# Kernel tuning notes

Hardware: AMD Instinct MI355X
Metric: run time of the kernel (lower is better)

The kernel has to match this reference:

```python
import jax, jax.numpy as jnp
import numpy as np

EPS = 1e-12  # matches torch F.normalize eps

def l2norm(x):
    n = jnp.linalg.norm(x, axis=-1, keepdims=True)
    return x / jnp.maximum(n, EPS)

def setup_inputs() -> dict:
    key = jax.random.key(0)
    ks = jax.random.split(key, 5)
    B, T, A, D, H = 32, 512, 64, 128, 256
    actions = jax.random.normal(ks[0], (B, T, A), dtype=jnp.float32)
    init_structure = jax.random.normal(ks[1], (D,), dtype=jnp.float32)
    # MLP params (scaled like typical init)
    w1 = jax.random.normal(ks[2], (A, H), dtype=jnp.float32) / jnp.sqrt(A)
    b1 = jnp.zeros((H,), dtype=jnp.float32)
    w2 = jax.random.normal(ks[3], (H, D * D), dtype=jnp.float32) / jnp.sqrt(H)
    b2 = jnp.zeros((D * D,), dtype=jnp.float32)
    return {"actions": actions, "init_structure": init_structure,
            "w1": w1, "b1": b1, "w2": w2, "b2": b2}

def reference(actions, init_structure, w1, b1, w2, b2):
    B, T, A = actions.shape
    D = init_structure.shape[0]
    # MLP: actions -> transition matrices [B, T, D, D]
    h = jax.nn.relu(jnp.einsum('bta,ah->bth', actions, w1) + b1)
    trans = (jnp.einsum('bth,hk->btk', h, w2) + b2).reshape(B, T, D, D)
    # initial structure, l2-normalized and broadcast over batch
    s0 = jnp.broadcast_to(l2norm(init_structure), (B, D))
    # sequential recurrence over time
    def step(s, Tm):  # s: [B, D], Tm: [B, D, D]
        s = jax.nn.relu(jnp.einsum('bi,bij->bj', s, Tm))
        s = l2norm(s)
        return s, s
    _, ys = jax.lax.scan(step, s0, jnp.swapaxes(trans, 0, 1))  # ys: [T, B, D]
    return jnp.swapaxes(ys, 0, 1)  # [B, T, D]
```

## Files before the change

### kernel.cpp

```cpp
#include <hip/hip_runtime.h>
#include <stdint.h>
#include <math.h>


typedef _Float16 f16x8 __attribute__((ext_vector_type(8)));
typedef float    f32x4 __attribute__((ext_vector_type(4)));

#define B_  32
#define T_  512
#define A_  64
#define H_  256
#define D_  128
#define N_  (D_ * D_)
#define M_  (B_ * T_)

__device__ inline void glds(const void* g, void* l) {
  __builtin_amdgcn_global_load_lds(
      (__attribute__((address_space(1))) void*)g,
      (__attribute__((address_space(3))) void*)l, 16, 0, 0);
}

__global__ __launch_bounds__(256) void w2cast_kernel(const float* __restrict__ w2,
                                                     _Float16* __restrict__ w2t) {
  __shared__ float tile[64][65];
  const int t = threadIdx.x;
  const int n0 = blockIdx.x * 64, k0 = blockIdx.y * 64;
  const int nn = t & 63, kg = t >> 6;
  #pragma unroll
  for (int r = 0; r < 16; ++r) {
    int k = kg * 16 + r;
    tile[k][nn] = w2[(size_t)(k0 + k) * N_ + n0 + nn];
  }
  __syncthreads();
  const int kk = t & 63, ng = t >> 6;
  #pragma unroll
  for (int r = 0; r < 16; ++r) {
    int n = ng * 16 + r;
    int ngl = n0 + n;
    int i = ngl >> 7, j = ngl & 127;
    int p = ((j >> 4) << 11) | ((i >> 5) << 9) | (((i >> 3) & 3) << 7)
          | ((j & 15) << 3) | (i & 7);
    w2t[(size_t)p * H_ + k0 + kk] = (_Float16)tile[kk][n];
  }
}

__global__ __launch_bounds__(256) void h_kernel(const float* __restrict__ actions,
                                                const float* __restrict__ w1,
                                                const float* __restrict__ b1,
                                                _Float16* __restrict__ h16) {
  __shared__ float w1s[32 * 256];
  __shared__ float acts[32 * 64];
  const int t = threadIdx.x;
  const size_t row0 = (size_t)blockIdx.x * 32;

  #pragma unroll
  for (int i = 0; i < 8; ++i) acts[t + i * 256] = actions[row0 * A_ + t + i * 256];

  float acc[32];
  float bj = b1[t];
  #pragma unroll
  for (int r = 0; r < 32; ++r) acc[r] = bj;

  for (int half = 0; half < 2; ++half) {
    __syncthreads();
    #pragma unroll
    for (int i = 0; i < 32; ++i) w1s[t + i * 256] = w1[half * 32 * 256 + t + i * 256];
    __syncthreads();
    #pragma unroll
    for (int r = 0; r < 32; ++r) {
      float a = acc[r];
      #pragma unroll
      for (int k = 0; k < 32; ++k)
        a += acts[r * 64 + half * 32 + k] * w1s[k * 256 + t];
      acc[r] = a;
    }
  }
  #pragma unroll
  for (int r = 0; r < 32; ++r)
    h16[(row0 + r) * H_ + t] = (_Float16)fmaxf(acc[r], 0.f);
}

__global__ __launch_bounds__(512, 2) void fused_kernel(
    const _Float16* __restrict__ h16, const _Float16* __restrict__ w2t,
    const float* __restrict__ b2, _Float16* __restrict__ tbuf0,
    _Float16* __restrict__ tbuf1, const float* __restrict__ init_s,
    float* __restrict__ out, float* __restrict__ dummyws,
    int Tc, int tcs, int c, int nch) {

  __shared__ __align__(16) char smem[33536];
  const int tid  = threadIdx.x;
  const int lane = tid & 63;
  const int w    = tid >> 6;

  if (blockIdx.x < 32) {
    if (c < 0) return;
    const char* trans = (const char*)((c & 1) ? tbuf1 : tbuf0);
    const int b  = blockIdx.x;
    const int t0 = c * Tc;
    const int n16 = lane & 15, q = lane >> 4;
    const int col = w * 16 + n16;
    const int Tcm1 = Tc - 1;
    float* red = (float*)(smem + 33280);
    _Float16* sb0p = (_Float16*)(smem + 32768);

    float v0 = 0.f;
    if (tid < 128) {
      v0 = (t0 == 0) ? init_s[tid] : out[((size_t)b * T_ + t0 - 1) * D_ + tid];
      float ss = v0 * v0;
      #pragma unroll
      for (int off = 32; off > 0; off >>= 1) ss += __shfl_xor(ss, off);
      if (lane == 0) red[w] = ss;
    }
    __syncthreads();
    if (tid < 128) {
      float inv0 = 1.f / fmaxf(sqrtf(red[0] + red[1]), 1e-12f);
      sb0p[tid] = (_Float16)(v0 * inv0);
    }
    __syncthreads();

    float uprev = (float)sb0p[col];

    const unsigned sbase = (unsigned)(size_t)(__attribute__((address_space(3))) char*)smem;
    const unsigned aA0 = sbase + 32768 + q * 16;
    const unsigned aA1 = sbase + 33024 + q * 16;
    const unsigned aW0 = sbase + 33024 + col * 2;
    const unsigned aW1 = sbase + 32768 + col * 2;
    const char* Gw = trans + (size_t)b * Tc * 32768 + w * 4096 + lane * 16;
    float* outb = out + (size_t)b * T_ * D_ + col;
    float* dsink = dummyws + blockIdx.x * 128 + col;

    f16x8 ring[4][4];
#define LDSLOT(S, P)                                                          \
    asm volatile("global_load_dwordx4 %0, %4, off\n\t"                        \
                 "global_load_dwordx4 %1, %4, off offset:1024\n\t"            \
                 "global_load_dwordx4 %2, %4, off offset:2048\n\t"            \
                 "global_load_dwordx4 %3, %4, off offset:3072"                \
                 : "=v"(ring[S][0]), "=v"(ring[S][1]),                        \
                   "=v"(ring[S][2]), "=v"(ring[S][3])                         \
                 : "v"(P) : "memory")
    LDSLOT(0, Gw + 0 * 32768);
    LDSLOT(1, Gw + 1 * 32768);
    LDSLOT(2, Gw + 2 * 32768);
    LDSLOT(3, Gw + 3 * 32768);

    const f32x4 zf = {0.f, 0.f, 0.f, 0.f};

#define STEP(TT, PAR, SPAR, WAITN)                                            \
    {                                                                         \
      const int tt = (TT);                                                    \
      f16x8 A0, A1, A2, A3;                                                   \
      asm volatile(                                                           \
        "s_waitcnt vmcnt(" #WAITN ")\n\t"                                     \
        "ds_read_b128 %0, %8 offset:0\n\t"                                    \
        "ds_read_b128 %1, %8 offset:64\n\t"                                   \
        "ds_read_b128 %2, %8 offset:128\n\t"                                  \
        "ds_read_b128 %3, %8 offset:192\n\t"                                  \
        "s_waitcnt lgkmcnt(0)"                                                \
        : "=v"(A0), "=v"(A1), "=v"(A2), "=v"(A3),                             \
          "+v"(ring[PAR][0]), "+v"(ring[PAR][1]),                             \
          "+v"(ring[PAR][2]), "+v"(ring[PAR][3])                              \
        : "v"(aA##SPAR) : "memory");                                          \
      f32x4 c0 = __builtin_amdgcn_mfma_f32_16x16x32_f16(A0, ring[PAR][0], zf, 0, 0, 0); \
      f32x4 c1 = __builtin_amdgcn_mfma_f32_16x16x32_f16(A1, ring[PAR][1], zf, 0, 0, 0); \
      f32x4 c2 = __builtin_amdgcn_mfma_f32_16x16x32_f16(A2, ring[PAR][2], zf, 0, 0, 0); \
      f32x4 c3 = __builtin_amdgcn_mfma_f32_16x16x32_f16(A3, ring[PAR][3], zf, 0, 0, 0); \
      f32x4 cs = __builtin_amdgcn_mfma_f32_16x16x32_f16(A0, A0, zf, 0, 0, 0); \
      cs = __builtin_amdgcn_mfma_f32_16x16x32_f16(A1, A1, cs, 0, 0, 0);       \
      cs = __builtin_amdgcn_mfma_f32_16x16x32_f16(A2, A2, cs, 0, 0, 0);       \
      cs = __builtin_amdgcn_mfma_f32_16x16x32_f16(A3, A3, cs, 0, 0, 0);       \
      const char* gd = Gw + (size_t)((tt + 4) & Tcm1) * 32768;                \
      LDSLOT(PAR, gd);                                                        \
      float ssp = cs[0];                                                      \
      float inv = 1.f / fmaxf(sqrtf(ssp), 1e-12f);                            \
      float y = c0[0] + c1[0] + c2[0] + c3[0];                                \
      float un = fmaxf(y, 0.f) * inv;                                         \
      float o = uprev * inv;                                                  \
      uprev = un;                                                             \
      _Float16 hv = (_Float16)un;                                             \
      const int gt = t0 + tt;                                                 \
      float* gp = (gt > 0) ? (outb + (size_t)(gt - 1) * D_) : dsink;          \
      asm volatile("ds_write_b16 %0, %1\n\t"                                  \
                   "global_store_dword %2, %3, off"                           \
                   :: "v"(aW##SPAR), "v"(hv), "v"(gp), "v"(o) : "memory");    \
      asm volatile("s_waitcnt lgkmcnt(0)\n\ts_barrier" ::: "memory");         \
    }

    STEP(0, 0, 0, 12)
    STEP(1, 1, 1, 13)
    STEP(2, 2, 0, 14)
    STEP(3, 3, 1, 15)
    for (int tt0 = 4; tt0 < Tc; tt0 += 4) {
      STEP(tt0,     0, 0, 16)
      STEP(tt0 + 1, 1, 1, 16)
      STEP(tt0 + 2, 2, 0, 16)
      STEP(tt0 + 3, 3, 1, 16)
    }
#undef STEP
#undef LDSLOT
    asm volatile("s_waitcnt vmcnt(0)" ::: "memory");

    {
      float x = 0.f;
      if (lane < 16) x = (float)((_Float16*)(smem + 32768))[col];
      float ss2 = x * x;
      ss2 += __shfl_xor(ss2, 1);
      ss2 += __shfl_xor(ss2, 2);
      ss2 += __shfl_xor(ss2, 4);
      ss2 += __shfl_xor(ss2, 8);
      if (lane == 0) red[w] = ss2;
      __syncthreads();
      float tot = 0.f;
      #pragma unroll
      for (int g = 0; g < 8; ++g) tot += red[g];
      float inv = 1.f / fmaxf(sqrtf(tot), 1e-12f);
      if (lane < 16) outb[(size_t)(t0 + Tc - 1) * D_] = uprev * inv;
    }
  } else {
    const int g = c + 1;
    if (g >= nch) return;
    _Float16* trans = (g & 1) ? tbuf1 : tbuf0;
    const int t0g = g * Tc;

    _Float16* smA = (_Float16*)smem;
    _Float16* smB = (_Float16*)(smem + 16384);

    const int wm = w >> 2, wn = w & 3;
    const int fm = lane & 15, fq = lane >> 4;
    const f32x4 zero = {0.f, 0.f, 0.f, 0.f};

    const int cA0 = tid, cA1 = tid + 512;
    const int rA0 = cA0 >> 2, kA0 = cA0 & 3;
    const int rA1 = cA1 >> 2, kA1 = cA1 & 3;

    const int mtiles = (B_ * Tc) >> 8;
    const int ntot = mtiles * 64;
    for (int tile = (int)blockIdx.x - 32; tile < ntot; tile += 224) {
      const int bn = tile & 63;
      const int bm = tile >> 6;

      const int mc0 = bm * 256 + rA0, mc1 = bm * 256 + rA1;
      const int bb0 = mc0 >> tcs, bb1 = mc1 >> tcs;
      const _Float16* gA0 = h16 + ((size_t)bb0 * T_ + t0g + (mc0 & (Tc - 1))) * H_ + kA0 * 8;
      const _Float16* gA1 = h16 + ((size_t)bb1 * T_ + t0g + (mc1 & (Tc - 1))) * H_ + kA1 * 8;
      const _Float16* gB0 = w2t + ((size_t)bn * 256 + rA0) * H_ + kA0 * 8;
      const _Float16* gB1 = w2t + ((size_t)bn * 256 + rA1) * H_ + kA1 * 8;
      _Float16* lA0 = &smA[cA0 * 8];
      _Float16* lA1 = &smA[cA1 * 8];
      _Float16* lB0 = &smB[cA0 * 8];
      _Float16* lB1 = &smB[cA1 * 8];

      f32x4 acc[8][4];
      #pragma unroll
      for (int i = 0; i < 8; ++i)
        #pragma unroll
        for (int j = 0; j < 4; ++j) acc[i][j] = zero;

      for (int kt = 0; kt < H_ / 32; ++kt) {
        __syncthreads();
        glds(gA0 + kt * 32, lA0);
        glds(gA1 + kt * 32, lA1);
        glds(gB0 + kt * 32, lB0);
        glds(gB1 + kt * 32, lB1);
        __syncthreads();
        f16x8 af[8], bf[4];
        #pragma unroll
        for (int mt = 0; mt < 8; ++mt)
          af[mt] = *(const f16x8*)&smA[(wm * 128 + mt * 16 + fm) * 32 + fq * 8];
        #pragma unroll
        for (int nt = 0; nt < 4; ++nt)
          bf[nt] = *(const f16x8*)&smB[(wn * 64 + nt * 16 + fm) * 32 + fq * 8];
        #pragma unroll
        for (int mt = 0; mt < 8; ++mt)
          #pragma unroll
          for (int nt = 0; nt < 4; ++nt)
            acc[mt][nt] = __builtin_amdgcn_mfma_f32_16x16x32_f16(af[mt], bf[nt], acc[mt][nt], 0, 0, 0);
      }

      #pragma unroll
      for (int nt = 0; nt < 4; ++nt) {
        int col = bn * 256 + wn * 64 + nt * 16 + fm;
        int pw = col >> 11, pf = (col >> 9) & 3, pq = (col >> 7) & 3;
        int pn = (col >> 3) & 15, pr = col & 7;
        int ii = pf * 32 + pq * 8 + pr, jj = pw * 16 + pn;
        float bias = b2[ii * 128 + jj];
        #pragma unroll
        for (int mt = 0; mt < 8; ++mt) {
          #pragma unroll
          for (int r = 0; r < 4; ++r) {
            long row = bm * 256 + wm * 128 + mt * 16 + fq * 4 + r;
            trans[row * (long)N_ + col] = (_Float16)(acc[mt][nt][r] + bias);
          }
        }
      }
      __syncthreads();
    }
  }
}

extern "C" void kernel_launch(void* const* d_in, const int* in_sizes, int n_in,
                              void* d_out, int out_size, void* d_ws, size_t ws_size,
                              hipStream_t stream) {
  const float* actions = (const float*)d_in[0];
  const float* init_s  = (const float*)d_in[1];
  const float* w1      = (const float*)d_in[2];
  const float* b1      = (const float*)d_in[3];
  const float* w2      = (const float*)d_in[4];
  const float* b2      = (const float*)d_in[5];
  float* out = (float*)d_out;

  uint8_t* ws = (uint8_t*)d_ws;
  _Float16* w2t = (_Float16*)ws;
  _Float16* h16 = (_Float16*)(ws + ((size_t)8 << 20));
  const size_t trans_off = (size_t)16 << 20;

  int Tc = 16;
  const int cands[3] = {64, 32, 16};
  for (int i = 0; i < 3; ++i) {
    if (trans_off + 2 * ((size_t)cands[i] << 20) + 65536 <= ws_size) { Tc = cands[i]; break; }
  }
  const int tcs = __builtin_ctz(Tc);
  _Float16* tbuf0 = (_Float16*)(ws + trans_off);
  _Float16* tbuf1 = (_Float16*)(ws + trans_off + ((size_t)Tc << 20));
  float* dummyws = (float*)(ws + trans_off + 2 * ((size_t)Tc << 20));

  w2cast_kernel<<<dim3(N_ / 64, 4), 256, 0, stream>>>(w2, w2t);
  h_kernel<<<M_ / 32, 256, 0, stream>>>(actions, w1, b1, h16);

  const int nch = T_ / Tc;
  for (int c = -1; c < nch; ++c) {
    fused_kernel<<<256, 512, 0, stream>>>(
        h16, w2t, b2, tbuf0, tbuf1, init_s, out, dummyws, Tc, tcs, c, nch);
  }
}
```

Before: 523.1 us.

## Replace per-chunk kernel launches with a persistent kernel using global flag synchronization

Collapses the loop of per-chunk fused_kernel launches into a single persistent launch. Recurrence blocks spin on per-group counters that the GEMM producer blocks increment once their tiles are written, and producers wait on consumer-done counters before reusing a double buffer. The aim is to remove launch gaps and the implicit grid-wide barrier between chunks, so producers can run ahead as far as the double buffer allows. In exchange it relies on all 256 blocks being co-resident and on correct memory fences, and spin-waiting adds polling overhead and deadlock risk.

```diff
diff --git a/kernel.cpp b/kernel.cpp
--- a/kernel.cpp
+++ b/kernel.cpp
@@ -21,7 +21,12 @@
 }
 
 __global__ __launch_bounds__(256) void w2cast_kernel(const float* __restrict__ w2,
-                                                     _Float16* __restrict__ w2t) {
+                                                     _Float16* __restrict__ w2t,
+                                                     unsigned* __restrict__ flags) {
+  if (blockIdx.x == 0 && blockIdx.y == 0) {
+    #pragma unroll
+    for (int i = 0; i < 4; ++i) flags[threadIdx.x + i * 256] = 0u;
+  }
   __shared__ float tile[64][65];
   const int t = threadIdx.x;
   const int n0 = blockIdx.x * 64, k0 = blockIdx.y * 64;
@@ -85,18 +90,16 @@
     const float* __restrict__ b2, _Float16* __restrict__ tbuf0,
     _Float16* __restrict__ tbuf1, const float* __restrict__ init_s,
     float* __restrict__ out, float* __restrict__ dummyws,
-    int Tc, int tcs, int c, int nch) {
+    unsigned* __restrict__ flags, int Tc, int tcs, int nch) {
 
   __shared__ __align__(16) char smem[33536];
   const int tid  = threadIdx.x;
   const int lane = tid & 63;
   const int w    = tid >> 6;
+  const int MT   = 1 << (tcs - 3);
 
   if (blockIdx.x < 32) {
-    if (c < 0) return;
-    const char* trans = (const char*)((c & 1) ? tbuf1 : tbuf0);
     const int b  = blockIdx.x;
-    const int t0 = c * Tc;
     const int n16 = lane & 15, q = lane >> 4;
     const int col = w * 16 + n16;
     const int Tcm1 = Tc - 1;
@@ -105,7 +108,7 @@
 
     float v0 = 0.f;
     if (tid < 128) {
-      v0 = (t0 == 0) ? init_s[tid] : out[((size_t)b * T_ + t0 - 1) * D_ + tid];
+      v0 = init_s[tid];
       float ss = v0 * v0;
       #pragma unroll
       for (int off = 32; off > 0; off >>= 1) ss += __shfl_xor(ss, off);
@@ -117,7 +120,6 @@
       sb0p[tid] = (_Float16)(v0 * inv0);
     }
     __syncthreads();
-
     float uprev = (float)sb0p[col];
 
     const unsigned sbase = (unsigned)(size_t)(__attribute__((address_space(3))) char*)smem;
@@ -125,11 +127,13 @@
     const unsigned aA1 = sbase + 33024 + q * 16;
     const unsigned aW0 = sbase + 33024 + col * 2;
     const unsigned aW1 = sbase + 32768 + col * 2;
-    const char* Gw = trans + (size_t)b * Tc * 32768 + w * 4096 + lane * 16;
     float* outb = out + (size_t)b * T_ * D_ + col;
-    float* dsink = dummyws + blockIdx.x * 128 + col;
+    float* dsink = dummyws + b * 128 + col;
+    const int grp = b >> (8 - tcs);
 
     f16x8 ring[4][4];
+    const f32x4 zf = {0.f, 0.f, 0.f, 0.f};
+
 #define LDSLOT(S, P)                                                          \
     asm volatile("global_load_dwordx4 %0, %4, off\n\t"                        \
                  "global_load_dwordx4 %1, %4, off offset:1024\n\t"            \
@@ -138,12 +142,6 @@
                  : "=v"(ring[S][0]), "=v"(ring[S][1]),                        \
                    "=v"(ring[S][2]), "=v"(ring[S][3])                         \
                  : "v"(P) : "memory")
-    LDSLOT(0, Gw + 0 * 32768);
-    LDSLOT(1, Gw + 1 * 32768);
-    LDSLOT(2, Gw + 2 * 32768);
-    LDSLOT(3, Gw + 3 * 32768);
-
-    const f32x4 zf = {0.f, 0.f, 0.f, 0.f};
 
 #define STEP(TT, PAR, SPAR, WAITN)                                            \
     {                                                                         \
@@ -185,19 +183,42 @@
       asm volatile("s_waitcnt lgkmcnt(0)\n\ts_barrier" ::: "memory");         \
     }
 
-    STEP(0, 0, 0, 12)
-    STEP(1, 1, 1, 13)
-    STEP(2, 2, 0, 14)
-    STEP(3, 3, 1, 15)
-    for (int tt0 = 4; tt0 < Tc; tt0 += 4) {
-      STEP(tt0,     0, 0, 16)
-      STEP(tt0 + 1, 1, 1, 16)
-      STEP(tt0 + 2, 2, 0, 16)
-      STEP(tt0 + 3, 3, 1, 16)
+    for (int c = 0; c < nch; ++c) {
+      if (tid == 0) {
+        while (__hip_atomic_load(&flags[c * MT + grp], __ATOMIC_RELAXED,
+                                 __HIP_MEMORY_SCOPE_AGENT) < 64u)
+          __builtin_amdgcn_s_sleep(8);
+        __threadfence();
+      }
+      __syncthreads();
+
+      const char* trans = (const char*)((c & 1) ? tbuf1 : tbuf0);
+      const char* Gw = trans + (size_t)b * Tc * 32768 + w * 4096 + lane * 16;
+      const int t0 = c * Tc;
+
+      LDSLOT(0, Gw + 0 * 32768);
+      LDSLOT(1, Gw + 1 * 32768);
+      LDSLOT(2, Gw + 2 * 32768);
+      LDSLOT(3, Gw + 3 * 32768);
+
+      STEP(0, 0, 0, 12)
+      STEP(1, 1, 1, 13)
+      STEP(2, 2, 0, 14)
+      STEP(3, 3, 1, 15)
+      for (int tt0 = 4; tt0 < Tc; tt0 += 4) {
+        STEP(tt0,     0, 0, 16)
+        STEP(tt0 + 1, 1, 1, 16)
+        STEP(tt0 + 2, 2, 0, 16)
+        STEP(tt0 + 3, 3, 1, 16)
+      }
+      asm volatile("s_waitcnt vmcnt(0)" ::: "memory");
+      __syncthreads();
+      if (tid == 0)
+        __hip_atomic_fetch_add(&flags[512 + c], 1u, __ATOMIC_RELAXED,
+                               __HIP_MEMORY_SCOPE_AGENT);
     }
 #undef STEP
 #undef LDSLOT
-    asm volatile("s_waitcnt vmcnt(0)" ::: "memory");
 
     {
       float x = 0.f;
@@ -213,14 +234,9 @@
       #pragma unroll
       for (int g = 0; g < 8; ++g) tot += red[g];
       float inv = 1.f / fmaxf(sqrtf(tot), 1e-12f);
-      if (lane < 16) outb[(size_t)(t0 + Tc - 1) * D_] = uprev * inv;
+      if (lane < 16) outb[(size_t)(T_ - 1) * D_] = uprev * inv;
     }
   } else {
-    const int g = c + 1;
-    if (g >= nch) return;
-    _Float16* trans = (g & 1) ? tbuf1 : tbuf0;
-    const int t0g = g * Tc;
-
     _Float16* smA = (_Float16*)smem;
     _Float16* smB = (_Float16*)(smem + 16384);
 
@@ -232,11 +248,26 @@
     const int rA0 = cA0 >> 2, kA0 = cA0 & 3;
     const int rA1 = cA1 >> 2, kA1 = cA1 & 3;
 
-    const int mtiles = (B_ * Tc) >> 8;
-    const int ntot = mtiles * 64;
-    for (int tile = (int)blockIdx.x - 32; tile < ntot; tile += 224) {
+    const int lnt = tcs + 3;
+    const int TOT = nch << lnt;
+
+    for (int job = (int)blockIdx.x - 32; job < TOT; job += 224) {
+      const int g    = job >> lnt;
+      const int tile = job & ((1 << lnt) - 1);
       const int bn = tile & 63;
       const int bm = tile >> 6;
+
+      if (g >= 2) {
+        if (tid == 0) {
+          while (__hip_atomic_load(&flags[512 + g - 2], __ATOMIC_RELAXED,
+                                   __HIP_MEMORY_SCOPE_AGENT) < 32u)
+            __builtin_amdgcn_s_sleep(8);
+        }
+        __syncthreads();
+      }
+
+      _Float16* trans = (g & 1) ? tbuf1 : tbuf0;
+      const int t0g = g * Tc;
 
       const int mc0 = bm * 256 + rA0, mc1 = bm * 256 + rA1;
       const int bb0 = mc0 >> tcs, bb1 = mc1 >> tcs;
@@ -293,6 +324,11 @@
         }
       }
       __syncthreads();
+      if (tid == 0) {
+        __threadfence();
+        __hip_atomic_fetch_add(&flags[g * MT + bm], 1u, __ATOMIC_RELAXED,
+                               __HIP_MEMORY_SCOPE_AGENT);
+      }
     }
   }
 }
@@ -316,19 +352,21 @@
   int Tc = 16;
   const int cands[3] = {64, 32, 16};
   for (int i = 0; i < 3; ++i) {
-    if (trans_off + 2 * ((size_t)cands[i] << 20) + 65536 <= ws_size) { Tc = cands[i]; break; }
+    if (trans_off + 2 * ((size_t)cands[i] << 20) + 65536 + 4096 <= ws_size) {
+      Tc = cands[i];
+      break;
+    }
   }
   const int tcs = __builtin_ctz(Tc);
   _Float16* tbuf0 = (_Float16*)(ws + trans_off);
   _Float16* tbuf1 = (_Float16*)(ws + trans_off + ((size_t)Tc << 20));
   float* dummyws = (float*)(ws + trans_off + 2 * ((size_t)Tc << 20));
-
-  w2cast_kernel<<<dim3(N_ / 64, 4), 256, 0, stream>>>(w2, w2t);
+  unsigned* flags = (unsigned*)(ws + trans_off + 2 * ((size_t)Tc << 20) + 65536);
+
+  w2cast_kernel<<<dim3(N_ / 64, 4), 256, 0, stream>>>(w2, w2t, flags);
   h_kernel<<<M_ / 32, 256, 0, stream>>>(actions, w1, b1, h16);
 
   const int nch = T_ / Tc;
-  for (int c = -1; c < nch; ++c) {
-    fused_kernel<<<256, 512, 0, stream>>>(
-        h16, w2t, b2, tbuf0, tbuf1, init_s, out, dummyws, Tc, tcs, c, nch);
-  }
-}
+  fused_kernel<<<256, 512, 0, stream>>>(h16, w2t, b2, tbuf0, tbuf1, init_s,
+                                        out, dummyws, flags, Tc, tcs, nch);
+}
```

Result: slower. 683.2 us (+30.6%).
